# Performance work log

Hardware: AMD Instinct MI355X
Metric: run time of the kernel (lower is better)

The kernel has to match this reference:

```python
import jax, jax.numpy as jnp
import numpy as np

NUM_HEADS = 8
LN_EPS = 1e-5
COS_EPS = 1e-8


def setup_inputs() -> dict:
    key = jax.random.key(0)
    ks = jax.random.split(key, 16)
    B, S, H, C = 16, 4096, 768, 64
    std = 0.02
    f32 = jnp.float32
    return {
        "hidden_states": jax.random.normal(ks[0], (B, S, H), f32),
        "concept_embeddings": jax.random.normal(ks[1], (C, H), f32),
        "Wq": jax.random.normal(ks[2], (H, H), f32) * std,
        "bq": jnp.zeros((H,), f32),
        "Wk": jax.random.normal(ks[3], (H, H), f32) * std,
        "bk": jnp.zeros((H,), f32),
        "Wv": jax.random.normal(ks[4], (H, H), f32) * std,
        "bv": jnp.zeros((H,), f32),
        "Wo": jax.random.normal(ks[5], (H, H), f32) * std,
        "bo": jnp.zeros((H,), f32),
        "Wg1": jax.random.normal(ks[6], (3 * H, H), f32) * std,
        "bg1": jnp.zeros((H,), f32),
        "Wg2": jax.random.normal(ks[7], (H, 1), f32) * std,
        "bg2": jnp.zeros((1,), f32),
        "ln_g": jnp.ones((H,), f32),
        "ln_b": jnp.zeros((H,), f32),
    }


def reference(hidden_states, concept_embeddings, Wq, bq, Wk, bk, Wv, bv,
              Wo, bo, Wg1, bg1, Wg2, bg2, ln_g, ln_b):
    B, S, H = hidden_states.shape
    C = concept_embeddings.shape[0]
    NH = NUM_HEADS
    HD = H // NH

    # QKV projections; concepts are shared across the batch
    Q = (hidden_states @ Wq + bq).reshape(B, S, NH, HD)      # [B,S,NH,HD]
    K = (concept_embeddings @ Wk + bk).reshape(C, NH, HD)    # [C,NH,HD]
    V = (concept_embeddings @ Wv + bv).reshape(C, NH, HD)

    scores = jnp.einsum('bshd,chd->bhsc', Q, K) / (HD ** 0.5)  # [B,NH,S,C]
    attn = jax.nn.softmax(scores, axis=-1)  # dropout is eval-mode identity
    context = jnp.einsum('bhsc,chd->bshd', attn, V).reshape(B, S, H)
    context = context @ Wo + bo

    # content relevance: cosine sim of mean-pooled text vs mean-pooled concepts
    text_pooled = hidden_states.mean(axis=1)          # [B,H]
    concept_pooled = concept_embeddings.mean(axis=0)  # [H] (same for all batch)
    num = text_pooled @ concept_pooled                # [B]
    den = jnp.maximum(jnp.linalg.norm(text_pooled, axis=-1), COS_EPS) * \
          jnp.maximum(jnp.linalg.norm(concept_pooled), COS_EPS)
    relevance = num / den                             # [B]
    rel_feat = jnp.broadcast_to(relevance[:, None, None], (B, S, H))

    gate_in = jnp.concatenate([hidden_states, context, rel_feat], axis=-1)  # [B,S,3H]
    gate = jax.nn.sigmoid(jax.nn.relu(gate_in @ Wg1 + bg1) @ Wg2 + bg2)     # [B,S,1]

    out = hidden_states + gate * context
    mu = out.mean(axis=-1, keepdims=True)
    var = out.var(axis=-1, keepdims=True)
    out = (out - mu) / jnp.sqrt(var + LN_EPS) * ln_g + ln_b

    attn_avg = attn.mean(axis=1)  # [B,S,C] for XAI
    return out, attn_avg
```

## Files before the change

### kernel.cpp

```cpp
#include <hip/hip_runtime.h>

typedef __attribute__((ext_vector_type(8))) short bf16x8;
typedef __attribute__((ext_vector_type(4))) float f32x4;
typedef unsigned short u16;

#define MFMA(a,b,c) __builtin_amdgcn_mfma_f32_16x16x32_bf16((a),(b),(c),0,0,0)

__device__ __forceinline__ short f2bf(float f){
  union { float f; unsigned u; } v; v.f = f;
  unsigned r = v.u + 0x7FFFu + ((v.u >> 16) & 1u);
  return (short)(r >> 16);
}
__device__ __forceinline__ float bf2f(short s){
  union { unsigned u; float f; } v; v.u = ((unsigned)(unsigned short)s) << 16; return v.f;
}
__device__ __forceinline__ bf16x8 pack8(f32x4 x, f32x4 y){
  bf16x8 r;
  r[0]=f2bf(x[0]); r[1]=f2bf(x[1]); r[2]=f2bf(x[2]); r[3]=f2bf(x[3]);
  r[4]=f2bf(y[0]); r[5]=f2bf(y[1]); r[6]=f2bf(y[2]); r[7]=f2bf(y[3]);
  return r;
}
__device__ __forceinline__ int pch(int c, int row){ return (c & ~7) | ((c & 7) ^ (row & 7)); }

__device__ __forceinline__ void gload16(void* lp, const void* gp){
  __builtin_amdgcn_global_load_lds((const __attribute__((address_space(1))) unsigned*)gp,
                                   (__attribute__((address_space(3))) unsigned*)lp, 16, 0, 0);
}
__device__ __forceinline__ void stWB(short* buf, const short* img, int half, int w, int lane){
  const char* gp = (const char*)img;
  #pragma unroll
  for (int it=0; it<4; ++it){
    int id = it*256 + w*64 + lane; int r = id>>3, c = id&7;
    gload16((char*)buf + it*4096 + w*1024, gp + r*256 + half*128 + c*16);
  }
}
__device__ __forceinline__ void stA128(short* buf, const u16* rowb, int kstep, int w, int lane){
  #pragma unroll
  for (int it=0; it<4; ++it){
    int id = it*256 + w*64 + lane; int r = id>>3, c = id&7;
    gload16((char*)buf + it*4096 + w*1024, rowb + (size_t)r*1536 + (kstep*8 + c)*8);
  }
}

__global__ void prep_w(const float* __restrict__ Wg1, short* __restrict__ WaI, short* __restrict__ WbI){
  __shared__ short lt[128][136];
  int blk = blockIdx.x;
  int mat = blk / 36, t = blk % 36, kt = t / 6, jt = t % 6;
  const float* src = (mat==0)? Wg1 : (Wg1 + (size_t)768*768);
  short* dst = (mat==0)? WaI : WbI;
  int tid = threadIdx.x;
  #pragma unroll
  for (int it=0; it<16; ++it){
    int kl = it*8 + (tid>>5);
    int jl = (tid&31)*4;
    f32x4 v = *(const f32x4*)&src[(size_t)(kt*128+kl)*768 + jt*128 + jl];
    lt[jl+0][kl]=f2bf(v[0]); lt[jl+1][kl]=f2bf(v[1]);
    lt[jl+2][kl]=f2bf(v[2]); lt[jl+3][kl]=f2bf(v[3]);
  }
  __syncthreads();
  size_t base = (size_t)(jt*6 + kt)*16384;
  #pragma unroll
  for (int cc=0; cc<8; ++cc){
    int ci = cc*256 + tid;
    int jl = ci >> 4, sc = ci & 15;
    int kkb = ((sc ^ (jl & 7)) << 3);
    bf16x8 v = *(const bf16x8*)&lt[jl][kkb];
    *(bf16x8*)&dst[base + (size_t)jl*128 + sc*8] = v;
  }
}

__global__ __launch_bounds__(256) void prep_kv(const float* __restrict__ ce,
                        const float* __restrict__ Wk, const float* __restrict__ bk,
                        const float* __restrict__ Wv, const float* __restrict__ bv,
                        short* __restrict__ Kc, short* __restrict__ VT){
  __shared__ float sh[8][768];
  int jt = blockIdx.x / 8, cg = blockIdx.x % 8;
  int tid = threadIdx.x;
  int j = jt*64 + (tid & 63);
  int cl = tid >> 6;
  for (int i = tid; i < 8*768; i += 256){
    int c2 = i / 768; int h = i - c2*768;
    sh[c2][h] = ce[(size_t)(cg*8+c2)*768 + h];
  }
  __syncthreads();
  float aK0=0.f, aV0=0.f, aK1=0.f, aV1=0.f;
  #pragma unroll 4
  for (int h=0; h<768; ++h){
    float wk = Wk[(size_t)h*768 + j];
    float wv = Wv[(size_t)h*768 + j];
    float x0 = sh[cl*2][h], x1 = sh[cl*2+1][h];
    aK0 += x0*wk; aV0 += x0*wv;
    aK1 += x1*wk; aV1 += x1*wv;
  }
  float bkj = bk[j], bvj = bv[j];
  int c0 = cg*8 + cl*2;
  Kc[(size_t)c0*768 + j]     = f2bf(aK0 + bkj);
  Kc[(size_t)(c0+1)*768 + j] = f2bf(aK1 + bkj);
  VT[(size_t)j*64 + c0]      = f2bf(aV0 + bvj);
  VT[(size_t)j*64 + c0+1]    = f2bf(aV1 + bvj);
}

__global__ void prep_misc(const float* __restrict__ Wg1, const float* __restrict__ ce,
                          const float* __restrict__ bq, const short* __restrict__ Kc,
                          float* __restrict__ wg1c, float* __restrict__ cp,
                          float* __restrict__ sbias){
  __shared__ float red[4][64];
  int b = blockIdx.x, tid = threadIdx.x;
  if (b < 12){
    int j = b*64 + (tid & 63);
    int kq = tid >> 6;
    float s = 0.f;
    for (int r=0; r<192; ++r)
      s += Wg1[(size_t)(1536 + kq*192 + r)*768 + j];
    red[kq][tid&63] = s;
    __syncthreads();
    if (tid < 64) wg1c[b*64+tid] = red[0][tid]+red[1][tid]+red[2][tid]+red[3][tid];
  } else if (b < 15){
    int h = (b-12)*256 + tid;
    float s = 0.f;
    #pragma unroll
    for (int c2=0; c2<64; ++c2) s += ce[(size_t)c2*768 + h];
    cp[h] = s * (1.f/64.f);
  } else {
    int hc = (b-15)*256 + tid;
    int h = hc >> 6, c = hc & 63;
    float s = 0.f;
    #pragma unroll
    for (int j=0; j<96; ++j)
      s += bq[h*96+j] * bf2f(Kc[(size_t)c*768 + h*96 + j]);
    sbias[hc] = s * 0.10206207262f;
  }
}

__global__ __launch_bounds__(256) void prep_eff(const float* __restrict__ Wq,
                        const short* __restrict__ Kc, short* __restrict__ WeffI){
  __shared__ short KA[64][104];
  __shared__ short WB[128][104];
  int h = blockIdx.x / 6, kt = blockIdx.x % 6, tid = threadIdx.x;
  const int lane = tid & 63, w = tid >> 6, l15 = lane & 15, g = lane >> 4;
  #pragma unroll
  for (int it=0; it<3; ++it){
    int i = it*256 + tid;
    int c = i / 12, cb = i % 12;
    *(bf16x8*)&KA[c][cb*8] = *(const bf16x8*)&Kc[(size_t)c*768 + h*96 + cb*8];
  }
  #pragma unroll
  for (int it=0; it<12; ++it){
    int i = it*256 + tid;
    int d = i / 24, q = i % 24;
    f32x4 v = *(const f32x4*)&Wq[(size_t)(kt*128+d)*768 + h*96 + q*4];
    WB[d][q*4+0]=f2bf(v[0]); WB[d][q*4+1]=f2bf(v[1]);
    WB[d][q*4+2]=f2bf(v[2]); WB[d][q*4+3]=f2bf(v[3]);
  }
  __syncthreads();
  f32x4 acc[4][2];
  #pragma unroll
  for (int i=0;i<4;++i){ acc[i][0]=(f32x4){0,0,0,0}; acc[i][1]=(f32x4){0,0,0,0}; }
  #pragma unroll
  for (int ks=0; ks<3; ++ks){
    bf16x8 a[4], b[2];
    #pragma unroll
    for (int mf=0; mf<4; ++mf) a[mf] = *(const bf16x8*)&KA[mf*16+l15][ks*32+g*8];
    #pragma unroll
    for (int nf=0; nf<2; ++nf) b[nf] = *(const bf16x8*)&WB[w*32+nf*16+l15][ks*32+g*8];
    #pragma unroll
    for (int mf=0; mf<4; ++mf)
      #pragma unroll
      for (int nf=0; nf<2; ++nf)
        acc[mf][nf] = MFMA(a[mf], b[nf], acc[mf][nf]);
  }
  size_t base = (size_t)((h>>1)*6 + kt)*16384;
  #pragma unroll
  for (int mf=0; mf<4; ++mf)
    #pragma unroll
    for (int nf=0; nf<2; ++nf)
      #pragma unroll
      for (int r=0; r<4; ++r){
        int c = mf*16 + g*4 + r;
        int d = w*32 + nf*16 + l15;
        int hcl = (h&1)*64 + c;
        WeffI[base + (size_t)hcl*128 + (((d>>3)^(hcl&7))<<3) + (d&7)] = f2bf(acc[mf][nf][r] * 0.10206207262f);
      }
}

__global__ __launch_bounds__(256) void prep_vwo(const float* __restrict__ Wo,
                        const short* __restrict__ VT, short* __restrict__ VWoI){
  __shared__ short WoT[128][104];
  __shared__ short VA[64][104];
  int h = blockIdx.x / 6, dt = blockIdx.x % 6, tid = threadIdx.x;
  const int lane = tid & 63, w = tid >> 6, l15 = lane & 15, g = lane >> 4;
  #pragma unroll
  for (int it=0; it<12; ++it){
    int i = it*256 + tid;
    int j = i / 32, qd = i % 32;
    f32x4 v = *(const f32x4*)&Wo[(size_t)(h*96+j)*768 + dt*128 + qd*4];
    WoT[qd*4+0][j]=f2bf(v[0]); WoT[qd*4+1][j]=f2bf(v[1]);
    WoT[qd*4+2][j]=f2bf(v[2]); WoT[qd*4+3][j]=f2bf(v[3]);
  }
  #pragma unroll
  for (int it=0; it<3; ++it){
    int i = it*256 + tid;
    int j = i / 8, cb = i % 8;
    bf16x8 v = *(const bf16x8*)&VT[(size_t)(h*96+j)*64 + cb*8];
    #pragma unroll
    for (int x=0; x<8; ++x) VA[cb*8+x][j] = v[x];
  }
  __syncthreads();
  f32x4 acc[2][4];
  #pragma unroll
  for (int i=0;i<2;++i)
    #pragma unroll
    for (int j=0;j<4;++j) acc[i][j]=(f32x4){0,0,0,0};
  #pragma unroll
  for (int ks=0; ks<3; ++ks){
    bf16x8 a[2], b[4];
    #pragma unroll
    for (int mf=0; mf<2; ++mf) a[mf] = *(const bf16x8*)&WoT[w*32+mf*16+l15][ks*32+g*8];
    #pragma unroll
    for (int nf=0; nf<4; ++nf) b[nf] = *(const bf16x8*)&VA[nf*16+l15][ks*32+g*8];
    #pragma unroll
    for (int mf=0; mf<2; ++mf)
      #pragma unroll
      for (int nf=0; nf<4; ++nf)
        acc[mf][nf] = MFMA(a[mf], b[nf], acc[mf][nf]);
  }
  size_t base = (size_t)(dt*4 + (h>>1))*16384;
  #pragma unroll
  for (int mf=0; mf<2; ++mf)
    #pragma unroll
    for (int nf=0; nf<4; ++nf)
      #pragma unroll
      for (int r=0; r<4; ++r){
        int d = w*32 + mf*16 + g*4 + r;
        int c = nf*16 + l15;
        int hcl = (h&1)*64 + c;
        VWoI[base + (size_t)d*128 + (((hcl>>3)^(d&7))<<3) + (hcl&7)] = f2bf(acc[mf][nf][r]);
      }
}

__global__ __launch_bounds__(384) void prep_hs(const float* __restrict__ hs,
                                               float* __restrict__ outp, float* __restrict__ tpp){
  __shared__ float csum[4][768];
  int tid = threadIdx.x;
  int c = tid % 96, rg = tid / 96;
  size_t r0 = (size_t)blockIdx.x * 128;
  u16* holes = (u16*)outp;
  float s[8];
  #pragma unroll
  for (int j=0;j<8;++j) s[j]=0.f;
  #pragma unroll 4
  for (int i=0; i<32; ++i){
    size_t row = r0 + rg*32 + i;
    const float* p = hs + row*768 + c*8;
    f32x4 x = __builtin_nontemporal_load((const f32x4*)p);
    f32x4 y = __builtin_nontemporal_load((const f32x4*)(p+4));
    *(bf16x8*)&holes[row*1536 + pch(c,(int)row)*8] = pack8(x,y);
    #pragma unroll
    for (int j=0;j<4;++j){ s[j]+=x[j]; s[4+j]+=y[j]; }
  }
  #pragma unroll
  for (int j=0;j<8;++j) csum[rg][c*8+j] = s[j];
  __syncthreads();
  for (int cc=tid; cc<768; cc+=384)
    tpp[(size_t)blockIdx.x*768 + cc] = csum[0][cc]+csum[1][cc]+csum[2][cc]+csum[3][cc];
}

__global__ void pool2(const float* __restrict__ tpp, float* __restrict__ tp){
  int b = blockIdx.x / 3, hc = blockIdx.x % 3;
  int h = hc*256 + threadIdx.x;
  float s = 0.f;
  #pragma unroll
  for (int k=0; k<32; ++k) s += tpp[((size_t)b*32 + k)*768 + h];
  tp[(size_t)b*768 + h] = s * (1.f/4096.f);
}
__global__ void pool3(const float* __restrict__ tp, const float* __restrict__ cp, float* __restrict__ rel){
  int b = blockIdx.x;
  float a=0.f, n1=0.f, n2=0.f;
  for (int h = threadIdx.x; h < 768; h += 256){
    float t = tp[(size_t)b*768 + h], c = cp[h];
    a += t*c; n1 += t*t; n2 += c*c;
  }
  #pragma unroll
  for (int m=1; m<64; m<<=1){ a+=__shfl_xor(a,m); n1+=__shfl_xor(n1,m); n2+=__shfl_xor(n2,m); }
  __shared__ float r3[3][4];
  int w = threadIdx.x >> 6;
  if ((threadIdx.x & 63) == 0){ r3[0][w]=a; r3[1][w]=n1; r3[2][w]=n2; }
  __syncthreads();
  if (threadIdx.x == 0){
    float A = r3[0][0]+r3[0][1]+r3[0][2]+r3[0][3];
    float N1= r3[1][0]+r3[1][1]+r3[1][2]+r3[1][3];
    float N2= r3[2][0]+r3[2][1]+r3[2][2]+r3[2][3];
    rel[b] = A / (fmaxf(sqrtf(N1),1e-8f) * fmaxf(sqrtf(N2),1e-8f));
  }
}

__global__ __launch_bounds__(256) void gs(const short* __restrict__ WeffI,
                                          const float* __restrict__ sbias, float* outp){
  __shared__ short A0[8192], A1[8192], B0[8192], B1[8192];
  const int tid = threadIdx.x, lane = tid & 63, w = tid >> 6;
  const int l15 = lane & 15, g = lane >> 4;
  const int bid = blockIdx.x;
  const int nb = (bid >> 3) & 3, mt = (bid/32)*8 + (bid & 7);
  const int wm = w & 1, wn = w >> 1;
  const size_t t0 = (size_t)mt*128;
  u16* holes = (u16*)outp;
  const u16* Arow = holes + t0*1536;
  const short* Wimg = WeffI + (size_t)nb*6*16384;
  f32x4 acc[4][4];
  #pragma unroll
  for (int i=0;i<4;++i)
    #pragma unroll
    for (int j=0;j<4;++j) acc[i][j] = (f32x4){0.f,0.f,0.f,0.f};
  stA128(A0, Arow, 0, w, lane);
  stWB(B0, Wimg, 0, w, lane);
  __syncthreads();
  #pragma unroll
  for (int ks2=0; ks2<12; ++ks2){
    const short* Ac = (ks2&1)? A1 : A0;
    const short* Bc = (ks2&1)? B1 : B0;
    short* An = (ks2&1)? A0 : A1;
    short* Bn = (ks2&1)? B0 : B1;
    if (ks2<11){
      stA128(An, Arow, ks2+1, w, lane);
      stWB(Bn, Wimg + (size_t)(((ks2+1)>>1))*16384, (ks2+1)&1, w, lane);
    }
    #pragma unroll
    for (int ks=0; ks<2; ++ks){
      bf16x8 a[4], b[4];
      #pragma unroll
      for (int mf=0; mf<4; ++mf){ int r = wm*64+mf*16+l15; a[mf] = *(const bf16x8*)&Ac[r*64 + (((ks*4+g)^(r&7))<<3)]; }
      #pragma unroll
      for (int nf=0; nf<4; ++nf){ int r = wn*64+nf*16+l15; b[nf] = *(const bf16x8*)&Bc[r*64 + (((ks*4+g)^(r&7))<<3)]; }
      #pragma unroll
      for (int mf=0; mf<4; ++mf)
        #pragma unroll
        for (int nf=0; nf<4; ++nf)
          acc[mf][nf] = MFMA(a[mf], b[nf], acc[mf][nf]);
    }
    __syncthreads();
  }
  #pragma unroll
  for (int mf=0; mf<4; ++mf)
    #pragma unroll
    for (int r=0; r<4; ++r){
      float v[4];
      #pragma unroll
      for (int nf=0; nf<4; ++nf)
        v[nf] = acc[mf][nf][r] + sbias[nb*128 + wn*64 + nf*16 + l15];
      float m = fmaxf(fmaxf(v[0],v[1]), fmaxf(v[2],v[3]));
      m = fmaxf(m,__shfl_xor(m,1)); m = fmaxf(m,__shfl_xor(m,2));
      m = fmaxf(m,__shfl_xor(m,4)); m = fmaxf(m,__shfl_xor(m,8));
      float e[4]; float s = 0.f;
      #pragma unroll
      for (int nf=0; nf<4; ++nf){ e[nf] = __expf(v[nf]-m); s += e[nf]; }
      s += __shfl_xor(s,1); s += __shfl_xor(s,2); s += __shfl_xor(s,4); s += __shfl_xor(s,8);
      float inv = 1.f/s;
      int grow = wm*64 + mf*16 + g*4 + r;
      #pragma unroll
      for (int nf=0; nf<4; ++nf){
        int col = nb*128 + wn*64 + nf*16 + l15;
        holes[(t0+grow)*1536 + 768 + pch(col>>3, grow)*8 + (col&7)] = (u16)f2bf(e[nf]*inv);
      }
    }
}

__global__ __launch_bounds__(256) void av(float* outp){
  const int tid = threadIdx.x, lane = tid & 63, w = tid >> 6;
  u16* holes = (u16*)outp;
  #pragma unroll 1
  for (int i=0; i<8; ++i){
    int row = i*8192 + blockIdx.x*4 + w;
    const u16* p = &holes[(size_t)row*1536 + 768 + pch(lane,row)*8];
    bf16x8 v = *(const bf16x8*)p;
    float x[8];
    #pragma unroll
    for (int j=0;j<8;++j) x[j] = bf2f(v[j]);
    #pragma unroll
    for (int j=0;j<8;++j){
      x[j] += __shfl_xor(x[j],8); x[j] += __shfl_xor(x[j],16); x[j] += __shfl_xor(x[j],32);
      x[j] *= 0.125f;
    }
    if (lane < 8){
      f32x4 o0, o1;
      #pragma unroll
      for (int j=0;j<4;++j){ o0[j]=x[j]; o1[j]=x[4+j]; }
      float* ap = &outp[(size_t)50331648 + (size_t)row*64 + lane*8];
      __builtin_nontemporal_store(o0, (f32x4*)ap);
      __builtin_nontemporal_store(o1, (f32x4*)(ap+4));
    }
  }
}

__global__ __launch_bounds__(256) void gvwo(const short* __restrict__ VWoI,
                                            const float* __restrict__ bo, float* outp){
  __shared__ short B0[8192], B1[8192];
  const int tid = threadIdx.x, lane = tid & 63, w = tid >> 6;
  const int l15 = lane & 15, g = lane >> 4;
  const size_t t0 = (size_t)blockIdx.x * 64;
  const int arow = w*16 + l15;
  const int drow = w*16 + g*4;
  u16* holes = (u16*)outp;
  bf16x8 af[16];
  #pragma unroll
  for (int kk=0; kk<16; ++kk){
    int kc = kk*4 + g;
    af[kk] = *(const bf16x8*)&holes[(t0+arow)*1536 + 768 + pch(kc, arow)*8];
  }
  stWB(B0, VWoI, 0, w, lane);
  __syncthreads();
  #pragma unroll 1
  for (int nb=0; nb<6; ++nb){
    f32x4 acc[8];
    #pragma unroll
    for (int i=0;i<8;++i) acc[i]=(f32x4){0.f,0.f,0.f,0.f};
    #pragma unroll
    for (int ks2=0; ks2<8; ++ks2){
      const short* Bc = (ks2&1)? B1 : B0;
      short* Bn = (ks2&1)? B0 : B1;
      if (ks2<7)       stWB(Bn, VWoI + (size_t)(nb*4 + ((ks2+1)>>1))*16384, (ks2+1)&1, w, lane);
      else if (nb<5)   stWB(Bn, VWoI + (size_t)((nb+1)*4)*16384, 0, w, lane);
      #pragma unroll
      for (int ks=0; ks<2; ++ks){
        bf16x8 a = af[ks2*2 + ks];
        #pragma unroll
        for (int nf=0; nf<8; ++nf){
          int br = nf*16 + l15;
          bf16x8 b = *(const bf16x8*)&Bc[br*64 + (((ks*4+g)^(br&7))<<3)];
          acc[nf] = MFMA(a, b, acc[nf]);
        }
      }
      __syncthreads();
    }
    #pragma unroll
    for (int nf=0; nf<8; ++nf)
      #pragma unroll
      for (int r=0; r<4; ++r){
        int row = drow + r;
        int col = nb*128 + nf*16 + l15;
        float v = acc[nf][r] + bo[col];
        holes[(t0+row)*1536 + 768 + pch(col>>3, row)*8 + (col&7)] = (u16)f2bf(v);
      }
  }
}

__global__ __launch_bounds__(256) void gate_mm(const short* __restrict__ WaI,
    const short* __restrict__ WbI, const float* __restrict__ bg1,
    const float* __restrict__ wg1c, const float* __restrict__ Wg2,
    const float* __restrict__ rel, float* __restrict__ gpart, float* outp){
  __shared__ short A0[8192], A1[8192], B0[8192], B1[8192];
  const int tid = threadIdx.x, lane = tid & 63, w = tid >> 6;
  const int l15 = lane & 15, g = lane >> 4;
  const int bid = blockIdx.x;
  const int nb = (bid >> 3) % 6, mt = (bid/48)*8 + (bid & 7);
  const int wm = w & 1, wn = w >> 1;
  const size_t t0 = (size_t)mt*128;
  const float relb = rel[t0 >> 12];
  u16* holes = (u16*)outp;
  const u16* h1p = holes + t0*1536;
  const u16* h2p = h1p + 768;
  f32x4 acc[4][4];
  #pragma unroll
  for (int i=0;i<4;++i)
    #pragma unroll
    for (int j=0;j<4;++j) acc[i][j]=(f32x4){0.f,0.f,0.f,0.f};
  stA128(A0, h1p, 0, w, lane);
  stWB(B0, WaI + (size_t)nb*6*16384, 0, w, lane);
  __syncthreads();
  #pragma unroll
  for (int pass=0; pass<2; ++pass){
    const short* Wimg = (pass? WbI : WaI) + (size_t)nb*6*16384;
    const u16* Ap = pass ? h2p : h1p;
    #pragma unroll
    for (int ks2=0; ks2<12; ++ks2){
      const short* Ac = (ks2&1)? A1 : A0;
      const short* Bc = (ks2&1)? B1 : B0;
      short* An = (ks2&1)? A0 : A1;
      short* Bn = (ks2&1)? B0 : B1;
      if (ks2<11){
        stA128(An, Ap, ks2+1, w, lane);
        stWB(Bn, Wimg + (size_t)(((ks2+1)>>1))*16384, (ks2+1)&1, w, lane);
      } else if (pass==0){
        stA128(An, h2p, 0, w, lane);
        stWB(Bn, WbI + (size_t)nb*6*16384, 0, w, lane);
      }
      #pragma unroll
      for (int ks=0; ks<2; ++ks){
        bf16x8 a[4], b[4];
        #pragma unroll
        for (int mf=0; mf<4; ++mf){ int r = wm*64+mf*16+l15; a[mf] = *(const bf16x8*)&Ac[r*64 + (((ks*4+g)^(r&7))<<3)]; }
        #pragma unroll
        for (int nf=0; nf<4; ++nf){ int r = wn*64+nf*16+l15; b[nf] = *(const bf16x8*)&Bc[r*64 + (((ks*4+g)^(r&7))<<3)]; }
        #pragma unroll
        for (int mf=0; mf<4; ++mf)
          #pragma unroll
          for (int nf=0; nf<4; ++nf)
            acc[mf][nf] = MFMA(a[mf], b[nf], acc[mf][nf]);
      }
      __syncthreads();
    }
  }
  float gp[4][4];
  #pragma unroll
  for (int mf=0; mf<4; ++mf)
    #pragma unroll
    for (int r=0; r<4; ++r) gp[mf][r]=0.f;
  #pragma unroll
  for (int mf=0; mf<4; ++mf)
    #pragma unroll
    for (int nf=0; nf<4; ++nf)
      #pragma unroll
      for (int r=0; r<4; ++r){
        int col = nb*128 + wn*64 + nf*16 + l15;
        gp[mf][r] += fmaxf(acc[mf][nf][r] + bg1[col] + relb*wg1c[col], 0.f) * Wg2[col];
      }
  #pragma unroll
  for (int mf=0; mf<4; ++mf)
    #pragma unroll
    for (int r=0; r<4; ++r){
      float v = gp[mf][r];
      v += __shfl_xor(v,1); v += __shfl_xor(v,2); v += __shfl_xor(v,4); v += __shfl_xor(v,8);
      gp[mf][r] = v;
    }
  __syncthreads();
  float* gred = (float*)B0;
  if (l15 == 0)
    #pragma unroll
    for (int mf=0; mf<4; ++mf)
      #pragma unroll
      for (int r=0; r<4; ++r)
        gred[wn*128 + wm*64 + mf*16 + g*4 + r] = gp[mf][r];
  __syncthreads();
  if (tid < 128)
    gpart[(size_t)nb*65536 + t0 + tid] = gred[tid] + gred[128+tid];
}

__global__ __launch_bounds__(256) void lnk(const float* __restrict__ gpart,
    const float* __restrict__ bg2, const float* __restrict__ lng,
    const float* __restrict__ lnb, float* outp){
  const int tid = threadIdx.x, lane = tid & 63, w = tid >> 6;
  u16* holes = (u16*)outp;
  const float bg2v = bg2[0];
  #pragma unroll 1
  for (int i=0; i<8; ++i){
    int row = blockIdx.x*32 + w*8 + i;
    float gsum = bg2v;
    #pragma unroll
    for (int nb2=0; nb2<6; ++nb2) gsum += gpart[(size_t)nb2*65536 + row];
    float gg = 1.f/(1.f + __expf(-gsum));
    int c1 = lane, c2 = 64 + (lane & 31);
    size_t rb = (size_t)row*1536;
    bf16x8 hv1 = *(const bf16x8*)&holes[rb + pch(c1,row)*8];
    bf16x8 ov1 = *(const bf16x8*)&holes[rb + 768 + pch(c1,row)*8];
    bf16x8 hv2 = *(const bf16x8*)&holes[rb + pch(c2,row)*8];
    bf16x8 ov2 = *(const bf16x8*)&holes[rb + 768 + pch(c2,row)*8];
    float x1[8], x2[8];
    float sum=0.f, sq=0.f;
    #pragma unroll
    for (int j=0;j<8;++j){ float x = bf2f(hv1[j]) + gg*bf2f(ov1[j]); x1[j]=x; sum+=x; sq+=x*x; }
    if (lane < 32){
      #pragma unroll
      for (int j=0;j<8;++j){ float x = bf2f(hv2[j]) + gg*bf2f(ov2[j]); x2[j]=x; sum+=x; sq+=x*x; }
    }
    #pragma unroll
    for (int m=1; m<64; m<<=1){ sum += __shfl_xor(sum,m); sq += __shfl_xor(sq,m); }
    float mu = sum * (1.f/768.f);
    float var = sq * (1.f/768.f) - mu*mu;
    float rs = rsqrtf(var + 1e-5f);
    {
      f32x4 ga = *(const f32x4*)&lng[c1*8], gb = *(const f32x4*)&lng[c1*8+4];
      f32x4 ba = *(const f32x4*)&lnb[c1*8], bb = *(const f32x4*)&lnb[c1*8+4];
      f32x4 o0, o1;
      #pragma unroll
      for (int j=0;j<4;++j){ o0[j] = (x1[j]-mu)*rs*ga[j]+ba[j]; o1[j] = (x1[4+j]-mu)*rs*gb[j]+bb[j]; }
      *(f32x4*)&outp[(size_t)row*768 + c1*8] = o0;
      *(f32x4*)&outp[(size_t)row*768 + c1*8 + 4] = o1;
    }
    if (lane < 32){
      f32x4 ga = *(const f32x4*)&lng[c2*8], gb = *(const f32x4*)&lng[c2*8+4];
      f32x4 ba = *(const f32x4*)&lnb[c2*8], bb = *(const f32x4*)&lnb[c2*8+4];
      f32x4 o0, o1;
      #pragma unroll
      for (int j=0;j<4;++j){ o0[j] = (x2[j]-mu)*rs*ga[j]+ba[j]; o1[j] = (x2[4+j]-mu)*rs*gb[j]+bb[j]; }
      *(f32x4*)&outp[(size_t)row*768 + c2*8] = o0;
      *(f32x4*)&outp[(size_t)row*768 + c2*8 + 4] = o1;
    }
  }
}

extern "C" void kernel_launch(void* const* d_in, const int* in_sizes, int n_in,
                              void* d_out, int out_size, void* d_ws, size_t ws_size,
                              hipStream_t stream) {
  (void)in_sizes; (void)n_in; (void)out_size; (void)ws_size;
  const float* hs  = (const float*)d_in[0];
  const float* ce  = (const float*)d_in[1];
  const float* Wq  = (const float*)d_in[2];
  const float* bq  = (const float*)d_in[3];
  const float* Wk  = (const float*)d_in[4];
  const float* bk  = (const float*)d_in[5];
  const float* Wv  = (const float*)d_in[6];
  const float* bv  = (const float*)d_in[7];
  const float* Wo  = (const float*)d_in[8];
  const float* bo  = (const float*)d_in[9];
  const float* Wg1 = (const float*)d_in[10];
  const float* bg1 = (const float*)d_in[11];
  const float* Wg2 = (const float*)d_in[12];
  const float* bg2 = (const float*)d_in[13];
  const float* lng = (const float*)d_in[14];
  const float* lnb = (const float*)d_in[15];
  char* ws = (char*)d_ws;
  short* WeffI = (short*)(ws + 0);
  short* VWoI  = (short*)(ws + 1179648);
  short* WaI   = (short*)(ws + 2359296);
  short* WbI   = (short*)(ws + 3538944);
  short* Kc    = (short*)(ws + 4718592);
  short* VT    = (short*)(ws + 4816896);
  float* wg1c  = (float*)(ws + 4915200);
  float* cp    = (float*)(ws + 4918272);
  float* tp    = (float*)(ws + 4921344);
  float* rel   = (float*)(ws + 4970496);
  float* tpp   = (float*)(ws + 4970752);
  float* gpart = (float*)(ws + 4970752);
  float* sbias = (float*)(ws + 6543616);
  float* outp  = (float*)d_out;

  prep_kv  <<<96,  256, 0, stream>>>(ce, Wk, bk, Wv, bv, Kc, VT);
  prep_w   <<<72,  256, 0, stream>>>(Wg1, WaI, WbI);
  prep_misc<<<17,  256, 0, stream>>>(Wg1, ce, bq, Kc, wg1c, cp, sbias);
  prep_eff <<<48,  256, 0, stream>>>(Wq, Kc, WeffI);
  prep_vwo <<<48,  256, 0, stream>>>(Wo, VT, VWoI);
  prep_hs  <<<512, 384, 0, stream>>>(hs, outp, tpp);
  pool2    <<<48,  256, 0, stream>>>(tpp, tp);
  pool3    <<<16,  256, 0, stream>>>(tp, cp, rel);
  gs       <<<2048,256, 0, stream>>>(WeffI, sbias, outp);
  av       <<<2048,256, 0, stream>>>(outp);
  gvwo     <<<1024,256, 0, stream>>>(VWoI, bo, outp);
  gate_mm  <<<3072,256, 0, stream>>>(WaI, WbI, bg1, wg1c, Wg2, rel, gpart, outp);
  lnk      <<<2048,256, 0, stream>>>(gpart, bg2, lng, lnb, outp);
}
```

Baseline: 538.6 us.

## Enlarge gate GEMM tiles to 256x256, fuse attn-average into gvwo, merge pooling kernels

The gate GEMM now runs 512-thread blocks that each compute a 256x256 output tile using 128KB of dynamic LDS, where it previously used 256-thread blocks with 128x128 tiles. This halves the number of column blocks and roughly halves re-reads of the A and B operands. The head-averaged attention output is now computed inside gvwo from the attention fragments it already holds in registers, which removes the separate av kernel and its extra read of the attention buffer. pool2 and pool3 are merged into a single kernel. The trade-offs are more register pressure per wave and lower occupancy, since only one large block fits per CU.

```diff
diff --git a/kernel.cpp b/kernel.cpp
--- a/kernel.cpp
+++ b/kernel.cpp
@@ -39,6 +39,23 @@
   for (int it=0; it<4; ++it){
     int id = it*256 + w*64 + lane; int r = id>>3, c = id&7;
     gload16((char*)buf + it*4096 + w*1024, rowb + (size_t)r*1536 + (kstep*8 + c)*8);
+  }
+}
+__device__ __forceinline__ void stA256(short* buf, const u16* rowb, int kstep, int w, int lane){
+  int tid = w*64 + lane;
+  #pragma unroll
+  for (int it=0; it<4; ++it){
+    int id = it*512 + tid; int r = id>>3, c = id&7;
+    gload16((char*)buf + it*8192 + w*1024, rowb + (size_t)r*1536 + (kstep*8 + c)*8);
+  }
+}
+__device__ __forceinline__ void stB256(short* buf, const short* img, int half, int w, int lane){
+  int tid = w*64 + lane;
+  #pragma unroll
+  for (int it=0; it<4; ++it){
+    int id = it*512 + tid; int r = id>>3, c = id&7;
+    gload16((char*)buf + it*8192 + w*1024,
+            img + (size_t)(r>>7)*98304 + (size_t)(r&127)*128 + half*64 + c*8);
   }
 }
 
@@ -265,20 +282,17 @@
     tpp[(size_t)blockIdx.x*768 + cc] = csum[0][cc]+csum[1][cc]+csum[2][cc]+csum[3][cc];
 }
 
-__global__ void pool2(const float* __restrict__ tpp, float* __restrict__ tp){
-  int b = blockIdx.x / 3, hc = blockIdx.x % 3;
-  int h = hc*256 + threadIdx.x;
-  float s = 0.f;
-  #pragma unroll
-  for (int k=0; k<32; ++k) s += tpp[((size_t)b*32 + k)*768 + h];
-  tp[(size_t)b*768 + h] = s * (1.f/4096.f);
-}
-__global__ void pool3(const float* __restrict__ tp, const float* __restrict__ cp, float* __restrict__ rel){
+__global__ void pool23(const float* __restrict__ tpp, const float* __restrict__ cp,
+                       float* __restrict__ rel){
   int b = blockIdx.x;
   float a=0.f, n1=0.f, n2=0.f;
   for (int h = threadIdx.x; h < 768; h += 256){
-    float t = tp[(size_t)b*768 + h], c = cp[h];
-    a += t*c; n1 += t*t; n2 += c*c;
+    float s = 0.f;
+    #pragma unroll
+    for (int k=0; k<32; ++k) s += tpp[((size_t)b*32 + k)*768 + h];
+    s *= (1.f/4096.f);
+    float c = cp[h];
+    a += s*c; n1 += s*s; n2 += c*c;
   }
   #pragma unroll
   for (int m=1; m<64; m<<=1){ a+=__shfl_xor(a,m); n1+=__shfl_xor(n1,m); n2+=__shfl_xor(n2,m); }
@@ -364,33 +378,6 @@
     }
 }
 
-__global__ __launch_bounds__(256) void av(float* outp){
-  const int tid = threadIdx.x, lane = tid & 63, w = tid >> 6;
-  u16* holes = (u16*)outp;
-  #pragma unroll 1
-  for (int i=0; i<8; ++i){
-    int row = i*8192 + blockIdx.x*4 + w;
-    const u16* p = &holes[(size_t)row*1536 + 768 + pch(lane,row)*8];
-    bf16x8 v = *(const bf16x8*)p;
-    float x[8];
-    #pragma unroll
-    for (int j=0;j<8;++j) x[j] = bf2f(v[j]);
-    #pragma unroll
-    for (int j=0;j<8;++j){
-      x[j] += __shfl_xor(x[j],8); x[j] += __shfl_xor(x[j],16); x[j] += __shfl_xor(x[j],32);
-      x[j] *= 0.125f;
-    }
-    if (lane < 8){
-      f32x4 o0, o1;
-      #pragma unroll
-      for (int j=0;j<4;++j){ o0[j]=x[j]; o1[j]=x[4+j]; }
-      float* ap = &outp[(size_t)50331648 + (size_t)row*64 + lane*8];
-      __builtin_nontemporal_store(o0, (f32x4*)ap);
-      __builtin_nontemporal_store(o1, (f32x4*)(ap+4));
-    }
-  }
-}
-
 __global__ __launch_bounds__(256) void gvwo(const short* __restrict__ VWoI,
                                             const float* __restrict__ bo, float* outp){
   __shared__ short B0[8192], B1[8192];
@@ -407,6 +394,33 @@
     af[kk] = *(const bf16x8*)&holes[(t0+arow)*1536 + 768 + pch(kc, arow)*8];
   }
   stWB(B0, VWoI, 0, w, lane);
+  {
+    float s0[8], s1[8];
+    #pragma unroll
+    for (int j=0;j<8;++j){ s0[j]=0.f; s1[j]=0.f; }
+    #pragma unroll
+    for (int kk=0; kk<16; kk+=2)
+      #pragma unroll
+      for (int j=0;j<8;++j) s0[j] += bf2f(af[kk][j]);
+    #pragma unroll
+    for (int kk=1; kk<16; kk+=2)
+      #pragma unroll
+      for (int j=0;j<8;++j) s1[j] += bf2f(af[kk][j]);
+    float* ap = &outp[(size_t)50331648 + (size_t)(t0+arow)*64];
+    f32x4 o;
+    #pragma unroll
+    for (int j=0;j<4;++j) o[j] = s0[j]*0.125f;
+    __builtin_nontemporal_store(o, (f32x4*)(ap + g*8));
+    #pragma unroll
+    for (int j=0;j<4;++j) o[j] = s0[4+j]*0.125f;
+    __builtin_nontemporal_store(o, (f32x4*)(ap + g*8 + 4));
+    #pragma unroll
+    for (int j=0;j<4;++j) o[j] = s1[j]*0.125f;
+    __builtin_nontemporal_store(o, (f32x4*)(ap + (4+g)*8));
+    #pragma unroll
+    for (int j=0;j<4;++j) o[j] = s1[4+j]*0.125f;
+    __builtin_nontemporal_store(o, (f32x4*)(ap + (4+g)*8 + 4));
+  }
   __syncthreads();
   #pragma unroll 1
   for (int nb=0; nb<6; ++nb){
@@ -443,32 +457,37 @@
   }
 }
 
-__global__ __launch_bounds__(256) void gate_mm(const short* __restrict__ WaI,
+__global__ void __launch_bounds__(512)
+__attribute__((amdgpu_waves_per_eu(2, 2))) gate_mm(const short* __restrict__ WaI,
     const short* __restrict__ WbI, const float* __restrict__ bg1,
     const float* __restrict__ wg1c, const float* __restrict__ Wg2,
     const float* __restrict__ rel, float* __restrict__ gpart, float* outp){
-  __shared__ short A0[8192], A1[8192], B0[8192], B1[8192];
+  extern __shared__ char lds[];
+  short* A0 = (short*)lds;
+  short* A1 = (short*)(lds + 32768);
+  short* B0 = (short*)(lds + 65536);
+  short* B1 = (short*)(lds + 98304);
   const int tid = threadIdx.x, lane = tid & 63, w = tid >> 6;
   const int l15 = lane & 15, g = lane >> 4;
   const int bid = blockIdx.x;
-  const int nb = (bid >> 3) % 6, mt = (bid/48)*8 + (bid & 7);
+  const int nb = (bid >> 3) % 3, mt = (bid/24)*8 + (bid & 7);
   const int wm = w & 1, wn = w >> 1;
-  const size_t t0 = (size_t)mt*128;
+  const size_t t0 = (size_t)mt*256;
   const float relb = rel[t0 >> 12];
   u16* holes = (u16*)outp;
   const u16* h1p = holes + t0*1536;
   const u16* h2p = h1p + 768;
-  f32x4 acc[4][4];
-  #pragma unroll
-  for (int i=0;i<4;++i)
+  f32x4 acc[8][4];
+  #pragma unroll
+  for (int i=0;i<8;++i)
     #pragma unroll
     for (int j=0;j<4;++j) acc[i][j]=(f32x4){0.f,0.f,0.f,0.f};
-  stA128(A0, h1p, 0, w, lane);
-  stWB(B0, WaI + (size_t)nb*6*16384, 0, w, lane);
-  __syncthreads();
-  #pragma unroll
+  stA256(A0, h1p, 0, w, lane);
+  stB256(B0, WaI + (size_t)(nb*2)*98304, 0, w, lane);
+  __syncthreads();
+  #pragma unroll 1
   for (int pass=0; pass<2; ++pass){
-    const short* Wimg = (pass? WbI : WaI) + (size_t)nb*6*16384;
+    const short* Wimg = pass ? (WbI + (size_t)(nb*2)*98304) : (WaI + (size_t)(nb*2)*98304);
     const u16* Ap = pass ? h2p : h1p;
     #pragma unroll
     for (int ks2=0; ks2<12; ++ks2){
@@ -477,21 +496,21 @@
       short* An = (ks2&1)? A0 : A1;
       short* Bn = (ks2&1)? B0 : B1;
       if (ks2<11){
-        stA128(An, Ap, ks2+1, w, lane);
-        stWB(Bn, Wimg + (size_t)(((ks2+1)>>1))*16384, (ks2+1)&1, w, lane);
+        stA256(An, Ap, ks2+1, w, lane);
+        stB256(Bn, Wimg + (size_t)((ks2+1)>>1)*16384, (ks2+1)&1, w, lane);
       } else if (pass==0){
-        stA128(An, h2p, 0, w, lane);
-        stWB(Bn, WbI + (size_t)nb*6*16384, 0, w, lane);
+        stA256(An, h2p, 0, w, lane);
+        stB256(Bn, WbI + (size_t)(nb*2)*98304, 0, w, lane);
       }
       #pragma unroll
       for (int ks=0; ks<2; ++ks){
-        bf16x8 a[4], b[4];
+        bf16x8 a[8], b[4];
         #pragma unroll
-        for (int mf=0; mf<4; ++mf){ int r = wm*64+mf*16+l15; a[mf] = *(const bf16x8*)&Ac[r*64 + (((ks*4+g)^(r&7))<<3)]; }
+        for (int mf=0; mf<8; ++mf){ int r = wm*128+mf*16+l15; a[mf] = *(const bf16x8*)&Ac[r*64 + (((ks*4+g)^(r&7))<<3)]; }
         #pragma unroll
         for (int nf=0; nf<4; ++nf){ int r = wn*64+nf*16+l15; b[nf] = *(const bf16x8*)&Bc[r*64 + (((ks*4+g)^(r&7))<<3)]; }
         #pragma unroll
-        for (int mf=0; mf<4; ++mf)
+        for (int mf=0; mf<8; ++mf)
           #pragma unroll
           for (int nf=0; nf<4; ++nf)
             acc[mf][nf] = MFMA(a[mf], b[nf], acc[mf][nf]);
@@ -499,39 +518,38 @@
       __syncthreads();
     }
   }
-  float gp[4][4];
-  #pragma unroll
-  for (int mf=0; mf<4; ++mf)
+  float gp[8][4];
+  #pragma unroll
+  for (int mf=0; mf<8; ++mf)
     #pragma unroll
     for (int r=0; r<4; ++r) gp[mf][r]=0.f;
   #pragma unroll
-  for (int mf=0; mf<4; ++mf)
+  for (int mf=0; mf<8; ++mf)
     #pragma unroll
     for (int nf=0; nf<4; ++nf)
       #pragma unroll
       for (int r=0; r<4; ++r){
-        int col = nb*128 + wn*64 + nf*16 + l15;
+        int col = nb*256 + wn*64 + nf*16 + l15;
         gp[mf][r] += fmaxf(acc[mf][nf][r] + bg1[col] + relb*wg1c[col], 0.f) * Wg2[col];
       }
   #pragma unroll
-  for (int mf=0; mf<4; ++mf)
+  for (int mf=0; mf<8; ++mf)
     #pragma unroll
     for (int r=0; r<4; ++r){
       float v = gp[mf][r];
       v += __shfl_xor(v,1); v += __shfl_xor(v,2); v += __shfl_xor(v,4); v += __shfl_xor(v,8);
       gp[mf][r] = v;
     }
-  __syncthreads();
-  float* gred = (float*)B0;
+  float* gred = (float*)lds;
   if (l15 == 0)
     #pragma unroll
-    for (int mf=0; mf<4; ++mf)
+    for (int mf=0; mf<8; ++mf)
       #pragma unroll
       for (int r=0; r<4; ++r)
-        gred[wn*128 + wm*64 + mf*16 + g*4 + r] = gp[mf][r];
-  __syncthreads();
-  if (tid < 128)
-    gpart[(size_t)nb*65536 + t0 + tid] = gred[tid] + gred[128+tid];
+        gred[wn*256 + wm*128 + mf*16 + g*4 + r] = gp[mf][r];
+  __syncthreads();
+  if (tid < 256)
+    gpart[(size_t)nb*65536 + t0 + tid] = gred[tid] + gred[256+tid] + gred[512+tid] + gred[768+tid];
 }
 
 __global__ __launch_bounds__(256) void lnk(const float* __restrict__ gpart,
@@ -545,7 +563,7 @@
     int row = blockIdx.x*32 + w*8 + i;
     float gsum = bg2v;
     #pragma unroll
-    for (int nb2=0; nb2<6; ++nb2) gsum += gpart[(size_t)nb2*65536 + row];
+    for (int nb2=0; nb2<3; ++nb2) gsum += gpart[(size_t)nb2*65536 + row];
     float gg = 1.f/(1.f + __expf(-gsum));
     int c1 = lane, c2 = 64 + (lane & 31);
     size_t rb = (size_t)row*1536;
@@ -616,7 +634,6 @@
   short* VT    = (short*)(ws + 4816896);
   float* wg1c  = (float*)(ws + 4915200);
   float* cp    = (float*)(ws + 4918272);
-  float* tp    = (float*)(ws + 4921344);
   float* rel   = (float*)(ws + 4970496);
   float* tpp   = (float*)(ws + 4970752);
   float* gpart = (float*)(ws + 4970752);
@@ -629,11 +646,11 @@
   prep_eff <<<48,  256, 0, stream>>>(Wq, Kc, WeffI);
   prep_vwo <<<48,  256, 0, stream>>>(Wo, VT, VWoI);
   prep_hs  <<<512, 384, 0, stream>>>(hs, outp, tpp);
-  pool2    <<<48,  256, 0, stream>>>(tpp, tp);
-  pool3    <<<16,  256, 0, stream>>>(tp, cp, rel);
+  pool23   <<<16,  256, 0, stream>>>(tpp, cp, rel);
   gs       <<<2048,256, 0, stream>>>(WeffI, sbias, outp);
-  av       <<<2048,256, 0, stream>>>(outp);
   gvwo     <<<1024,256, 0, stream>>>(VWoI, bo, outp);
-  gate_mm  <<<3072,256, 0, stream>>>(WaI, WbI, bg1, wg1c, Wg2, rel, gpart, outp);
+  hipFuncSetAttribute(reinterpret_cast<const void*>(gate_mm),
+                      hipFuncAttributeMaxDynamicSharedMemorySize, 131072);
+  gate_mm  <<<768, 512, 131072, stream>>>(WaI, WbI, bg1, wg1c, Wg2, rel, gpart, outp);
   lnk      <<<2048,256, 0, stream>>>(gpart, bg2, lng, lnb, outp);
 }
```

New measurement: 503.9 us. 1.07x faster.
